# Kernel optimization log

Measured on AMD Instinct MI355X. Metric: run time of the kernel, lower is better.

The kernel has to match this reference:

```python
import jax
jax.config.update("jax_enable_x64", True)
import jax.numpy as jnp
from jax import lax
import numpy as np

SR, LOWER, UPPER, ORDER = 16000, 500, 7000, 8


def _butter_bandpass_ba(N, lower, upper, sr):
    """Replicates scipy.signal.butter(N, [2*lo/sr, 2*hi/sr], 'bandpass')."""
    Wn = np.array([2.0 * lower / sr, 2.0 * upper / sr])
    fs = 2.0
    warped = 2.0 * fs * np.tan(np.pi * Wn / fs)  # pre-warp for bilinear
    # analog Butterworth lowpass prototype (buttap)
    m = np.arange(-N + 1, N, 2)
    p = -np.exp(1j * np.pi * m / (2 * N))
    k = 1.0
    # lp2bp_zpk
    bw = warped[1] - warped[0]
    wo = np.sqrt(warped[0] * warped[1])
    degree = len(p)  # no finite zeros in prototype
    p_lp = p * bw / 2.0
    p_bp = np.concatenate([p_lp + np.sqrt(p_lp ** 2 - wo ** 2),
                           p_lp - np.sqrt(p_lp ** 2 - wo ** 2)])
    z_bp = np.zeros(degree, dtype=complex)
    k_bp = k * bw ** degree
    # bilinear_zpk (fs=2)
    fs2 = 2.0 * fs
    z_d = (fs2 + z_bp) / (fs2 - z_bp)
    p_d = (fs2 + p_bp) / (fs2 - p_bp)
    z_d = np.append(z_d, -np.ones(len(p_bp) - len(z_bp)))
    k_d = k_bp * np.real(np.prod(fs2 - z_bp) / np.prod(fs2 - p_bp))
    b = np.real(k_d * np.poly(z_d))
    a = np.real(np.poly(p_d))
    return b, a


def _lfilter_zi(b, a):
    """Replicates scipy.signal.lfilter_zi (steady-state of step response)."""
    n = len(a)
    comp = np.zeros((n - 1, n - 1))
    comp[0, :] = -a[1:] / a[0]
    comp[1:, :-1] = np.eye(n - 2)
    IminusA = np.eye(n - 1) - comp.T
    B = b[1:] - a[1:] * b[0]
    return np.linalg.solve(IminusA, B)


def _lfilter(b, a, x, zi):
    """Direct-form II transposed IIR filter. x: [B, L], zi: [B, n-1]."""
    b0, bt, at = b[0], b[1:], a[1:]

    def step(z, xt):  # z: [B, n-1], xt: [B]
        y = b0 * xt + z[:, 0]
        z_shift = jnp.concatenate([z[:, 1:], jnp.zeros_like(z[:, :1])], axis=1)
        z_new = z_shift + xt[:, None] * bt[None, :] - y[:, None] * at[None, :]
        return z_new, y

    _, y = lax.scan(step, zi, x.T)
    return y.T


def _filtfilt(b, a, x):
    """Replicates scipy.signal.filtfilt defaults (padtype='odd', method='pad')."""
    padlen = 3 * max(len(a), len(b))
    # odd extension along time
    left = 2.0 * x[:, :1] - x[:, 1:padlen + 1][:, ::-1]
    right = 2.0 * x[:, -1:] - x[:, -padlen - 1:-1][:, ::-1]
    ext = jnp.concatenate([left, x, right], axis=1)
    zi = jnp.asarray(_lfilter_zi(b, a))[None, :]  # [1, n-1]
    bj, aj = jnp.asarray(b), jnp.asarray(a)
    y = _lfilter(bj, aj, ext, zi * ext[:, :1])          # forward pass
    yr = y[:, ::-1]
    y = _lfilter(bj, aj, yr, zi * yr[:, :1])            # backward pass
    y = y[:, ::-1]
    return y[:, padlen:-padlen]


def setup_inputs() -> dict:
    key = jax.random.key(0)
    audio = jax.random.normal(key, (32, 262144), dtype=jnp.float32)
    return {"audio": audio}


def reference(audio) -> jnp.ndarray:
    b, a = _butter_bandpass_ba(ORDER, LOWER, UPPER, SR)
    y = _filtfilt(b, a, audio.astype(jnp.float64))
    return y.astype(jnp.float32)
```

## Files before the change

kernel.cpp:

```cpp
#include <hip/hip_runtime.h>
#include <cmath>
#include <complex>

#define NB    32
#define LX    262144
#define PAD   51
#define LTOT  (LX + 2 * PAD)
#define CM    16
#define F_PAD 1946
#define LPAD  (LTOT + F_PAD)
#define TILE  (64 * CM)
#define NTILE (LPAD / TILE)
#define WPB   4
#define NBX   ((NTILE + WPB - 1) / WPB)
#define NP    8
#define LDSR  17
#define WIN   14
#define WREG  1280

struct CoeffsS { float a1[NP], a2[NP], b0[NP], b1[NP], c0; };
struct LvS { float lv[6][NP][4]; };

__device__ __forceinline__ void wave_sync() {
    asm volatile("s_waitcnt lgkmcnt(0)" ::: "memory");
}

__global__ void k_init(float4* __restrict__ mt, LvS L) {
    int id = blockIdx.x * 256 + threadIdx.x;
    if (id >= 512) return;
    int t = id >> 3, q = id & 7;
    float m0 = 1.f, m1 = 0.f, m2 = 0.f, m3 = 1.f;
    for (int k = 0; k < 6; k++)
        if ((t >> k) & 1) {
            float a0 = L.lv[k][q][0], a1 = L.lv[k][q][1];
            float a2 = L.lv[k][q][2], a3 = L.lv[k][q][3];
            float n0 = a0 * m0 + a1 * m2, n1 = a0 * m1 + a1 * m3;
            float n2 = a2 * m0 + a3 * m2, n3 = a2 * m1 + a3 * m3;
            m0 = n0; m1 = n1; m2 = n2; m3 = n3;
        }
    mt[id] = make_float4(m0, m1, m2, m3);
}

__device__ __forceinline__ void load_uA(const float* __restrict__ x,
                                        float base, int c, float (&u)[CM]) {
    int t0 = c * CM - F_PAD;
    if (t0 >= PAD && t0 + CM <= PAD + LX) {
        const float* xs = x + (t0 - PAD);
#pragma unroll
        for (int m = 0; m < CM / 4; m++) {
            float4 v = *reinterpret_cast<const float4*>(xs + 4 * m);
            u[4 * m] = v.x - base; u[4 * m + 1] = v.y - base;
            u[4 * m + 2] = v.z - base; u[4 * m + 3] = v.w - base;
        }
    } else {
#pragma unroll
        for (int i = 0; i < CM; i++) {
            int t = t0 + i;
            float uu;
            if (t < 0) uu = 0.f;
            else {
                float e;
                if (t < PAD)            e = 2.0f * x[0] - x[PAD - t];
                else if (t < PAD + LX)  e = x[t - PAD];
                else                    e = 2.0f * x[LX - 1] - x[2 * LX + PAD - 2 - t];
                uu = e - base;
            }
            u[i] = uu;
        }
    }
}

__device__ __forceinline__ void load_uB(const float* __restrict__ yb,
                                        float base, int c, float (&u)[CM]) {
    if (c < 0) {
#pragma unroll
        for (int i = 0; i < CM; i++) u[i] = 0.f;
        return;
    }
    const float* ys = yb + (size_t)c * CM;
#pragma unroll
    for (int m = 0; m < CM / 4; m++) {
        float4 v = *reinterpret_cast<const float4*>(ys + 4 * m);
        u[4 * m] = v.x - base; u[4 * m + 1] = v.y - base;
        u[4 * m + 2] = v.z - base; u[4 * m + 3] = v.w - base;
    }
}

__device__ __forceinline__ void local_states(const float (&u)[CM], const CoeffsS& C,
                                             float (&w1)[NP], float (&w2)[NP]) {
#pragma unroll
    for (int q = 0; q < NP; q++) { w1[q] = 0.f; w2[q] = 0.f; }
#pragma unroll
    for (int i = 0; i < CM; i++) {
        float uu = u[i];
#pragma unroll
        for (int q = 0; q < NP; q++) {
            float wt = fmaf(C.a1[q], w1[q], fmaf(C.a2[q], w2[q], uu));
            w2[q] = w1[q]; w1[q] = wt;
        }
    }
}

__device__ __forceinline__ void pack_states(float4* sc4, int j,
                                            const float (&w1)[NP], const float (&w2)[NP]) {
#pragma unroll
    for (int p = 0; p < 4; p++)
        sc4[p * 80 + j] = make_float4(w1[2 * p], w2[2 * p], w1[2 * p + 1], w2[2 * p + 1]);
}

template <int PASS>
__global__ __launch_bounds__(256) void k_full(const float* __restrict__ in,
                                              float* __restrict__ outp,
                                              const float4* __restrict__ mt,
                                              CoeffsS C) {
    __shared__ __align__(16) float lds[WPB * WREG];
    int tid = threadIdx.x, wv = tid >> 6, l = tid & 63;
    int ttx = blockIdx.x * WPB + wv, b = blockIdx.y;
    if (ttx >= NTILE) return;
    int c = ttx * 64 + l;
    float* wlds = lds + wv * WREG;
    float4* sc4 = reinterpret_cast<float4*>(wlds);

    const float* x = in + (size_t)b * (PASS == 0 ? LX : LPAD);
    float base = (PASS == 0) ? (2.0f * x[0] - x[PAD]) : x[0];

    if (l < WIN) {
        float uw[CM];
        int cw = ttx * 64 - WIN + l;
        if (PASS == 0) load_uA(x, base, cw, uw);
        else           load_uB(x, base, cw, uw);
        float w1[NP], w2[NP];
        local_states(uw, C, w1, w2);
        pack_states(sc4, l, w1, w2);
    }

    float u[CM];
    if (PASS == 0) load_uA(x, base, c, u);
    else           load_uB(x, base, c, u);
    float w1[NP], w2[NP];
    local_states(u, C, w1, w2);
    pack_states(sc4, WIN + l, w1, w2);
    wave_sync();

    float e1[NP], e2[NP];
#pragma unroll
    for (int q = 0; q < NP; q++) { e1[q] = 0.f; e2[q] = 0.f; }
#pragma unroll
    for (int k = 1; k <= WIN; k++) {
#pragma unroll
        for (int p = 0; p < 4; p++) {
            float4 f = sc4[p * 80 + WIN + l - k];
            float4 ma = mt[(k - 1) * NP + 2 * p];
            float4 mb = mt[(k - 1) * NP + 2 * p + 1];
            e1[2 * p]     = fmaf(ma.x, f.x, fmaf(ma.y, f.y, e1[2 * p]));
            e2[2 * p]     = fmaf(ma.z, f.x, fmaf(ma.w, f.y, e2[2 * p]));
            e1[2 * p + 1] = fmaf(mb.x, f.z, fmaf(mb.y, f.w, e1[2 * p + 1]));
            e2[2 * p + 1] = fmaf(mb.z, f.z, fmaf(mb.w, f.w, e2[2 * p + 1]));
        }
    }

#pragma unroll
    for (int q = 0; q < NP; q++) { w1[q] = e1[q]; w2[q] = e2[q]; }
#pragma unroll
    for (int i = 0; i < CM; i++) {
        float uu = u[i];
        float y = C.c0 * uu;
#pragma unroll
        for (int q = 0; q < NP; q++) {
            float wt = fmaf(C.a1[q], w1[q], fmaf(C.a2[q], w2[q], uu));
            y = fmaf(C.b0[q], wt, fmaf(C.b1[q], w1[q], y));
            w2[q] = w1[q]; w1[q] = wt;
        }
        u[i] = y;
    }

    wave_sync();
#pragma unroll
    for (int i = 0; i < CM; i++) wlds[l * LDSR + i] = u[i];
    wave_sync();

    if (PASS == 0) {
        float4* yb4 = reinterpret_cast<float4*>(
            outp + (size_t)b * LPAD + (size_t)(NTILE - 1 - ttx) * TILE);
#pragma unroll
        for (int k = 0; k < 4; k++) {
            int o4 = l + 64 * k;
            int ts = 63 - (o4 >> 2);
            int ih = 15 - 4 * (o4 & 3);
            const float* r = &wlds[ts * LDSR];
            yb4[o4] = make_float4(r[ih], r[ih - 1], r[ih - 2], r[ih - 3]);
        }
    } else {
        float* ob = outp + (size_t)b * LX;
        int J0 = (LTOT - 1 - PAD) - ttx * TILE;
#pragma unroll
        for (int it = 0; it < CM; it++) {
            int o = it * 64 + l;
            int j = J0 - o;
            if (j >= 0 && j < LX)
                ob[j] = wlds[(o >> 4) * LDSR + (o & 15)];
        }
    }
}

static void compute_coeffs(CoeffsS& C, LvS& L) {
    using cd = std::complex<double>;
    const int N = 8;
    const double sr = 16000.0, lo = 500.0, hi = 7000.0, fs = 2.0;
    double w0 = 2.0 * fs * std::tan(M_PI * (2.0 * lo / sr) / fs);
    double w1 = 2.0 * fs * std::tan(M_PI * (2.0 * hi / sr) / fs);
    double bw = w1 - w0, wo = std::sqrt(w0 * w1);
    cd pbp[16];
    for (int k = 0; k < N; k++) {
        int m = -N + 1 + 2 * k;
        cd pl = -std::exp(cd(0.0, M_PI * m / (2.0 * N)));
        pl *= bw / 2.0;
        cd s = std::sqrt(pl * pl - cd(wo * wo, 0.0));
        pbp[k] = pl + s; pbp[k + N] = pl - s;
    }
    double kbp = std::pow(bw, (double)N);
    const double fs2 = 4.0;
    cd pd[16], denom = 1.0;
    for (int i = 0; i < 16; i++) {
        pd[i] = (cd(fs2, 0.0) + pbp[i]) / (cd(fs2, 0.0) - pbp[i]);
        denom *= (cd(fs2, 0.0) - pbp[i]);
    }
    double kd = kbp * std::real(cd(std::pow(fs2, 8.0), 0.0) / denom);
    cd prodp = 1.0;
    for (int i = 0; i < 16; i++) prodp *= pd[i];
    cd c0 = cd(kd, 0.0) / prodp;
    int n = 0;
    for (int i = 0; i < 16; i++) {
        if (pd[i].imag() <= 0.0) continue;
        cd inv = 1.0 / pd[i];
        cd t1 = cd(1.0, 0.0) - inv, t2 = cd(1.0, 0.0) + inv;
        cd numr = cd(kd, 0.0);
        for (int k = 0; k < 8; k++) numr *= t1;
        for (int k = 0; k < 8; k++) numr *= t2;
        cd den = 1.0;
        for (int j = 0; j < 16; j++)
            if (j != i) den *= (cd(1.0, 0.0) - pd[j] * inv);
        cd r2 = 2.0 * numr / den;
        if (n < NP) {
            double a1 = 2.0 * pd[i].real();
            double a2 = -std::norm(pd[i]);
            C.a1[n] = (float)a1; C.a2[n] = (float)a2;
            C.b0[n] = (float)r2.real();
            C.b1[n] = (float)(-(r2.real() * pd[i].real() + r2.imag() * pd[i].imag()));
            double M[4] = { a1, a2, 1.0, 0.0 };
            for (int s = 0; s < 4; s++) {
                double q0 = M[0] * M[0] + M[1] * M[2], q1 = M[0] * M[1] + M[1] * M[3];
                double q2 = M[2] * M[0] + M[3] * M[2], q3 = M[2] * M[1] + M[3] * M[3];
                M[0] = q0; M[1] = q1; M[2] = q2; M[3] = q3;
            }
            for (int k = 0; k < 6; k++) {
                for (int j = 0; j < 4; j++) L.lv[k][n][j] = (float)M[j];
                double q0 = M[0] * M[0] + M[1] * M[2], q1 = M[0] * M[1] + M[1] * M[3];
                double q2 = M[2] * M[0] + M[3] * M[2], q3 = M[2] * M[1] + M[3] * M[3];
                M[0] = q0; M[1] = q1; M[2] = q2; M[3] = q3;
            }
            n++;
        }
    }
    C.c0 = (float)c0.real();
}

extern "C" void kernel_launch(void* const* d_in, const int* in_sizes, int n_in,
                              void* d_out, int out_size, void* d_ws, size_t ws_size,
                              hipStream_t stream) {
    const float* audio = (const float*)d_in[0];
    float* out = (float*)d_out;

    CoeffsS C; LvS L;
    compute_coeffs(C, L);

    char* ws = (char*)d_ws;
    size_t o = 0;
    auto alloc = [&](size_t bytes) { size_t r = o; o += (bytes + 255) & ~(size_t)255; return r; };
    float*  ybuf = (float*)(ws + alloc((size_t)NB * LPAD * sizeof(float)));
    float4* mt   = (float4*)(ws + alloc(512 * sizeof(float4)));

    dim3 blk(256), g(NBX, NB);

    k_init   <<<2, 256, 0, stream>>>(mt, L);
    k_full<0><<<g, blk, 0, stream>>>(audio, ybuf, mt, C);
    k_full<1><<<g, blk, 0, stream>>>(ybuf, out, mt, C);
}
```

Baseline: 64.73 us.

## Replace windowed LDS state combination with shuffle-based Kogge-Stone prefix scan

The per-lane carry-in state used to be built by summing 14 neighbouring lanes' local states, each multiplied by a transfer matrix. That required staging all lane states in LDS and doing 14 unrolled matrix-vector steps per lane. Now a 4-step Kogge-Stone scan using wavefront shuffles and per-level transfer matrices runs inside the wave. Only the first 16 lanes still add the contribution from the preceding window out of LDS. This cuts LDS traffic and FMA work, but adds shuffle latency, a divergent loop on the low lanes, and a longer window that is still truncated.

```diff
diff --git a/kernel.cpp b/kernel.cpp
--- a/kernel.cpp
+++ b/kernel.cpp
@@ -15,8 +15,8 @@
 #define NBX   ((NTILE + WPB - 1) / WPB)
 #define NP    8
 #define LDSR  17
-#define WIN   14
-#define WREG  1280
+#define WIN   16
+#define WREG  1088
 
 struct CoeffsS { float a1[NP], a2[NP], b0[NP], b1[NP], c0; };
 struct LvS { float lv[6][NP][4]; };
@@ -101,25 +101,18 @@
     }
 }
 
-__device__ __forceinline__ void pack_states(float4* sc4, int j,
-                                            const float (&w1)[NP], const float (&w2)[NP]) {
-#pragma unroll
-    for (int p = 0; p < 4; p++)
-        sc4[p * 80 + j] = make_float4(w1[2 * p], w2[2 * p], w1[2 * p + 1], w2[2 * p + 1]);
-}
-
 template <int PASS>
 __global__ __launch_bounds__(256) void k_full(const float* __restrict__ in,
                                               float* __restrict__ outp,
                                               const float4* __restrict__ mt,
-                                              CoeffsS C) {
+                                              CoeffsS C, LvS L) {
     __shared__ __align__(16) float lds[WPB * WREG];
     int tid = threadIdx.x, wv = tid >> 6, l = tid & 63;
     int ttx = blockIdx.x * WPB + wv, b = blockIdx.y;
     if (ttx >= NTILE) return;
     int c = ttx * 64 + l;
     float* wlds = lds + wv * WREG;
-    float4* sc4 = reinterpret_cast<float4*>(wlds);
+    float4* scw = reinterpret_cast<float4*>(wlds);
 
     const float* x = in + (size_t)b * (PASS == 0 ? LX : LPAD);
     float base = (PASS == 0) ? (2.0f * x[0] - x[PAD]) : x[0];
@@ -131,45 +124,67 @@
         else           load_uB(x, base, cw, uw);
         float w1[NP], w2[NP];
         local_states(uw, C, w1, w2);
-        pack_states(sc4, l, w1, w2);
+#pragma unroll
+        for (int p = 0; p < 4; p++)
+            scw[p * WIN + l] = make_float4(w1[2 * p], w2[2 * p],
+                                           w1[2 * p + 1], w2[2 * p + 1]);
     }
 
     float u[CM];
     if (PASS == 0) load_uA(x, base, c, u);
     else           load_uB(x, base, c, u);
-    float w1[NP], w2[NP];
-    local_states(u, C, w1, w2);
-    pack_states(sc4, WIN + l, w1, w2);
+    float g1[NP], g2[NP];
+    local_states(u, C, g1, g2);
+
+#pragma unroll
+    for (int s = 0; s < 4; s++) {
+        int d = 1 << s;
+#pragma unroll
+        for (int q = 0; q < NP; q++) {
+            float o1 = __shfl_up(g1[q], d);
+            float o2 = __shfl_up(g2[q], d);
+            if (l < d) { o1 = 0.f; o2 = 0.f; }
+            g1[q] = fmaf(L.lv[s][q][0], o1, fmaf(L.lv[s][q][1], o2, g1[q]));
+            g2[q] = fmaf(L.lv[s][q][2], o1, fmaf(L.lv[s][q][3], o2, g2[q]));
+        }
+    }
+
+    float e1[NP], e2[NP];
+#pragma unroll
+    for (int q = 0; q < NP; q++) {
+        float a = __shfl_up(g1[q], 1), bb = __shfl_up(g2[q], 1);
+        e1[q] = (l == 0) ? 0.f : a;
+        e2[q] = (l == 0) ? 0.f : bb;
+    }
+
     wave_sync();
-
-    float e1[NP], e2[NP];
-#pragma unroll
-    for (int q = 0; q < NP; q++) { e1[q] = 0.f; e2[q] = 0.f; }
-#pragma unroll
-    for (int k = 1; k <= WIN; k++) {
-#pragma unroll
-        for (int p = 0; p < 4; p++) {
-            float4 f = sc4[p * 80 + WIN + l - k];
-            float4 ma = mt[(k - 1) * NP + 2 * p];
-            float4 mb = mt[(k - 1) * NP + 2 * p + 1];
-            e1[2 * p]     = fmaf(ma.x, f.x, fmaf(ma.y, f.y, e1[2 * p]));
-            e2[2 * p]     = fmaf(ma.z, f.x, fmaf(ma.w, f.y, e2[2 * p]));
-            e1[2 * p + 1] = fmaf(mb.x, f.z, fmaf(mb.y, f.w, e1[2 * p + 1]));
-            e2[2 * p + 1] = fmaf(mb.z, f.z, fmaf(mb.w, f.w, e2[2 * p + 1]));
-        }
-    }
-
-#pragma unroll
-    for (int q = 0; q < NP; q++) { w1[q] = e1[q]; w2[q] = e2[q]; }
+    if (l < WIN) {
+        for (int j = l; j < WIN; j++) {
+            int km1 = WIN - 1 + l - j;
+#pragma unroll
+            for (int p = 0; p < 4; p++) {
+                float4 fw = scw[p * WIN + j];
+                float4 ma = mt[km1 * NP + 2 * p];
+                float4 mb = mt[km1 * NP + 2 * p + 1];
+                e1[2 * p]     = fmaf(ma.x, fw.x, fmaf(ma.y, fw.y, e1[2 * p]));
+                e2[2 * p]     = fmaf(ma.z, fw.x, fmaf(ma.w, fw.y, e2[2 * p]));
+                e1[2 * p + 1] = fmaf(mb.x, fw.z, fmaf(mb.y, fw.w, e1[2 * p + 1]));
+                e2[2 * p + 1] = fmaf(mb.z, fw.z, fmaf(mb.w, fw.w, e2[2 * p + 1]));
+            }
+        }
+    }
+
+#pragma unroll
+    for (int q = 0; q < NP; q++) { g1[q] = e1[q]; g2[q] = e2[q]; }
 #pragma unroll
     for (int i = 0; i < CM; i++) {
         float uu = u[i];
         float y = C.c0 * uu;
 #pragma unroll
         for (int q = 0; q < NP; q++) {
-            float wt = fmaf(C.a1[q], w1[q], fmaf(C.a2[q], w2[q], uu));
-            y = fmaf(C.b0[q], wt, fmaf(C.b1[q], w1[q], y));
-            w2[q] = w1[q]; w1[q] = wt;
+            float wt = fmaf(C.a1[q], g1[q], fmaf(C.a2[q], g2[q], uu));
+            y = fmaf(C.b0[q], wt, fmaf(C.b1[q], g1[q], y));
+            g2[q] = g1[q]; g1[q] = wt;
         }
         u[i] = y;
     }
@@ -283,6 +298,6 @@
     dim3 blk(256), g(NBX, NB);
 
     k_init   <<<2, 256, 0, stream>>>(mt, L);
-    k_full<0><<<g, blk, 0, stream>>>(audio, ybuf, mt, C);
-    k_full<1><<<g, blk, 0, stream>>>(ybuf, out, mt, C);
-}
+    k_full<0><<<g, blk, 0, stream>>>(audio, ybuf, mt, C, L);
+    k_full<1><<<g, blk, 0, stream>>>(ybuf, out, mt, C, L);
+}
```

After: 73.95 us. 1.14x slower.
